# Kernel optimization log

Hardware: AMD Instinct MI355X
Metric: run time of the kernel (lower is better)

## Reference

```python
import jax, jax.numpy as jnp
import numpy as np

S, B, DIN = 3, 4096, 1024
H1, H2, H3, D = 512, 384, 256, 128
K, C = 512, 3            # codebook size, n_codebooks
TEMP = 0.1               # contrastive temperature
EPS = 1e-12


def setup_inputs() -> dict:
    key = jax.random.key(0)
    ks = jax.random.split(key, 16)
    g = lambda k, shp, s=0.05: (jax.random.normal(k, shp, dtype=jnp.float32) * s)
    return {
        'x': jax.random.normal(ks[0], (S, B, DIN), dtype=jnp.float32),
        'enc_w1': g(ks[1], (S, DIN, H1)), 'enc_b1': g(ks[2], (S, H1)),
        'enc_w2': g(ks[3], (S, H1, H2)), 'enc_b2': g(ks[4], (S, H2)),
        'enc_w3': g(ks[5], (S, H2, H3)), 'enc_b3': g(ks[6], (S, H3)),
        'enc_w4': g(ks[7], (S, H3, D)),  'enc_b4': g(ks[8], (S, D)),
        'q_w1': g(ks[9], (D, D)), 'q_b1': g(ks[10], (D,)),
        'q_w2': g(ks[11], (D,)),
        'codebooks': jax.random.normal(ks[12], (C, K, D), dtype=jnp.float32),
    }


def _normalize(v):
    return v / jnp.maximum(jnp.linalg.norm(v, axis=-1, keepdims=True), EPS)


def _forward(x, enc_w1, enc_b1, enc_w2, enc_b2, enc_w3, enc_b3,
             enc_w4, enc_b4, q_w1, q_b1, q_w2, codebooks):
    sg = jax.lax.stop_gradient
    # per-source MLP encoders (stacked over source axis s)
    h = jax.nn.relu(jnp.einsum('sbi,sio->sbo', x, enc_w1) + enc_b1[:, None, :])
    h = jax.nn.relu(jnp.einsum('sbi,sio->sbo', h, enc_w2) + enc_b2[:, None, :])
    h = jax.nn.relu(jnp.einsum('sbi,sio->sbo', h, enc_w3) + enc_b3[:, None, :])
    emb = jnp.einsum('sbi,sio->sbo', h, enc_w4) + enc_b4[:, None, :]  # [S,B,D]

    # attention fusion: Linear->Tanh->Linear(1) per source, softmax over sources
    score = jnp.einsum('sbd,d->sb', jnp.tanh(jnp.einsum('sbd,de->sbe', emb, q_w1) + q_b1), q_w2)
    weight = jax.nn.softmax(score.T, axis=-1)                # [B,S]
    fused = jnp.einsum('bs,sbd->bd', weight, emb)            # [B,D]

    # residual VQ over C codebooks (straight-through, MSE losses)
    res = fused
    q_sum = jnp.zeros_like(fused)
    commit_loss = jnp.float32(0.0)
    for k in range(C):
        e = codebooks[k]                                     # [K,D]
        d2 = (jnp.sum(res * res, axis=1, keepdims=True)
              - 2.0 * res @ e.T + jnp.sum(e * e, axis=1))    # [B,K]
        ids = jnp.argmin(d2, axis=1)
        q = e[ids]                                           # [B,D]
        commit_loss = commit_loss + jnp.mean((sg(q) - res) ** 2)
        q_st = res + sg(q - res)                             # straight-through
        q_sum = q_sum + q_st
        res = res - q_st

    # codebook regularizer: mean pairwise cosine gram of normalized codebooks
    cbn = _normalize(codebooks)
    codebook_loss = jnp.mean(jnp.einsum('mkd,mjd->mkj', cbn, cbn))

    # contrastive losses (projection = identity)
    z1 = _normalize(q_sum)                                   # [B,D]
    contrast = []
    for s in range(S):
        z2 = _normalize(emb[s])
        refl = jnp.exp((z1 @ z1.T) / TEMP)                   # [B,B]
        between = jnp.exp((z1 @ z2.T) / TEMP)
        pos = jnp.diagonal(between)
        denom = refl.sum(1) + between.sum(1) - jnp.diagonal(refl)
        contrast.append(jnp.mean(-jnp.log(pos / denom)))

    return jnp.stack([1.0 * codebook_loss, 0.0 * commit_loss] + contrast)


def reference(x, enc_w1, enc_b1, enc_w2, enc_b2, enc_w3, enc_b3,
              enc_w4, enc_b4, q_w1, q_b1, q_w2, codebooks):
    return _forward(x, enc_w1, enc_b1, enc_w2, enc_b2, enc_w3, enc_b3,
                    enc_w4, enc_b4, q_w1, q_b1, q_w2, codebooks)
```

## Files before the change

### kernel.cpp

```cpp
#include <hip/hip_runtime.h>
#include <hip/hip_bf16.h>

#define S_   3
#define B_   4096
#define DIN_ 1024
#define H1_  512
#define H2_  384
#define H3_  256
#define D_   128
#define K_   512
#define C_   3
#define INV_T 10.0f
#define EPS_  1e-12f
#define EXP10 22026.465794806718f

typedef float f32x4 __attribute__((ext_vector_type(4)));
typedef short bf16x8 __attribute__((ext_vector_type(8)));

__device__ __forceinline__ unsigned short f2bf(float f) {
  unsigned int u = __float_as_uint(f);
  u = (u + 0x7FFF + ((u >> 16) & 1)) >> 16;
  return (unsigned short)u;
}

__device__ __forceinline__ void gl2lds16(const unsigned short* g, unsigned short* l) {
  __builtin_amdgcn_global_load_lds(
      (const __attribute__((address_space(1))) void*)g,
      (__attribute__((address_space(3))) void*)l, 16, 0, 0);
}

__device__ __forceinline__ float waveReduceSum(float v) {
#pragma unroll
  for (int off = 32; off > 0; off >>= 1) v += __shfl_down(v, off, 64);
  return v;
}

__device__ __forceinline__ float waveXorSum(float v) {
#pragma unroll
  for (int off = 32; off > 0; off >>= 1) v += __shfl_xor(v, off, 64);
  return v;
}

__global__ __launch_bounds__(256) void prep_kernel(
    const float* __restrict__ x, unsigned short* __restrict__ xb,
    const float* __restrict__ w1, unsigned short* __restrict__ wt1,
    const float* __restrict__ w2, unsigned short* __restrict__ wt2,
    const float* __restrict__ w3, unsigned short* __restrict__ wt3,
    const float* __restrict__ w4, unsigned short* __restrict__ wt4,
    const float* __restrict__ cb, float* __restrict__ cbn2,
    float* __restrict__ cbsumP, unsigned short* __restrict__ cbb,
    const float* __restrict__ qw1, unsigned short* __restrict__ qw1tb) {
  __shared__ float tt[32][33];
  __shared__ float invn[64];
  const int t = threadIdx.x;
  int blk = blockIdx.x;
  const int NCVT = (S_ * B_ * DIN_) / 1024;
  if (blk < NCVT) {
    int i = (blk * 256 + t) * 4;
    float4 v = *(const float4*)(x + i);
    xb[i + 0] = f2bf(v.x); xb[i + 1] = f2bf(v.y);
    xb[i + 2] = f2bf(v.z); xb[i + 3] = f2bf(v.w);
    return;
  }
  blk -= NCVT;
  const int NT = 1536 + 576 + 288 + 96;
  if (blk >= NT) {
    int cblk = blk - NT;
    if (cblk < 24) {
      const int m = cblk >> 3;
      const int k0 = (cblk & 7) * 64;
      const int w = t >> 6, lane = t & 63;
      for (int r = w * 16; r < w * 16 + 16; r++) {
        int k = k0 + r;
        float2 v = *(const float2*)(cb + ((size_t)m * K_ + k) * D_ + lane * 2);
        unsigned short* crow = cbb + ((size_t)m * K_ + k) * D_;
        crow[lane * 2 + 0] = f2bf(v.x);
        crow[lane * 2 + 1] = f2bf(v.y);
        float n2 = waveXorSum(v.x * v.x + v.y * v.y);
        if (lane == 0) {
          cbn2[m * K_ + k] = n2;
          invn[r] = 1.0f / fmaxf(sqrtf(n2), EPS_);
        }
      }
      __syncthreads();
      if (t < D_) {
        float acc = 0.0f;
        for (int r = 0; r < 64; r++)
          acc += cb[((size_t)m * K_ + k0 + r) * D_ + t] * invn[r];
        cbsumP[(size_t)cblk * D_ + t] = acc;
      }
      return;
    }
    cblk -= 24;
    const int kx = cblk & 3, ny = cblk >> 2;
    const int k0 = kx * 32, n0 = ny * 32;
    const int tx = t & 31, ty = t >> 5;
#pragma unroll
    for (int i = 0; i < 4; i++)
      tt[ty + 8 * i][tx] = qw1[(size_t)(k0 + ty + 8 * i) * D_ + n0 + tx];
    __syncthreads();
#pragma unroll
    for (int i = 0; i < 4; i++)
      qw1tb[(size_t)(n0 + ty + 8 * i) * D_ + k0 + tx] = f2bf(tt[tx][ty + 8 * i]);
    return;
  }
  const float* W; unsigned short* Wt; int K, N;
  if (blk < 1536) { W = w1; Wt = wt1; K = DIN_; N = H1_; }
  else {
    blk -= 1536;
    if (blk < 576) { W = w2; Wt = wt2; K = H1_; N = H2_; }
    else {
      blk -= 576;
      if (blk < 288) { W = w3; Wt = wt3; K = H2_; N = H3_; }
      else { blk -= 288; W = w4; Wt = wt4; K = H3_; N = D_; }
    }
  }
  const int kx_n = K / 32, ny_n = N / 32;
  const int kx = blk % kx_n;
  const int ny = (blk / kx_n) % ny_n;
  const int s  = blk / (kx_n * ny_n);
  const int k0 = kx * 32, n0 = ny * 32;
  const int tx = t & 31, ty = t >> 5;
  const float* Ws = W + (size_t)s * K * N;
  const int nb = N >> 7, kb = K >> 6;
#pragma unroll
  for (int i = 0; i < 4; i++)
    tt[ty + 8 * i][tx] = Ws[(size_t)(k0 + ty + 8 * i) * N + n0 + tx];
  __syncthreads();
  const int k = k0 + tx;
  const int kt = k >> 6, ksl = (k >> 5) & 1;
#pragma unroll
  for (int i = 0; i < 4; i++) {
    int n = n0 + ty + 8 * i;
    size_t dst = ((size_t)(s * nb + (n >> 7)) * kb + kt) * 8192 +
                 (size_t)ksl * 4096 + (size_t)(n & 127) * 32 + (k & 31);
    Wt[dst] = f2bf(tt[tx][ty + 8 * i]);
  }
}

__global__ __launch_bounds__(256) void gemm_lds_kernel(
    const unsigned short* __restrict__ A, const unsigned short* __restrict__ Wsw,
    const float* __restrict__ bias, void* __restrict__ Y,
    int K, int N, int relu, int out_f32) {
  const int t = threadIdx.x;
  const int lane = t & 63;
  const int w = t >> 6;
  const int ln = lane & 15, q = lane >> 4;
  const int wm = w >> 1, wn = w & 1;
  const int n0 = blockIdx.x * 128;
  const int mblk = blockIdx.y;
  const int s = mblk >> 6;
  const int m0 = mblk * 64;
  const int nb = N >> 7, kb = K >> 6;

  const unsigned short* Ag = A + (size_t)m0 * K;
  const unsigned short* Bt = Wsw + ((size_t)(s * nb + blockIdx.x) * kb) * 8192;
  const float* bs = bias + (size_t)s * N;

  __shared__ unsigned short Asm[2 * 64 * 32];
  __shared__ unsigned short Bsm[2 * 8192];

  const int arow0 = t >> 3, ak8 = t & 7;
  const int aL0 = (ak8 >> 2) * 2048 + arow0 * 32 + (ak8 & 3) * 8;
  const size_t gA0 = (size_t)arow0 * K + ak8 * 8;

  bf16x8 ra0 = *(const bf16x8*)(Ag + gA0);
  bf16x8 ra1 = *(const bf16x8*)(Ag + gA0 + (size_t)32 * K);
#pragma unroll
  for (int p = 0; p < 4; p++)
    gl2lds16(Bt + (size_t)(p * 256 + t) * 8, &Bsm[(size_t)(p * 256 + t) * 8]);

  f32x4 acc[2][4];
#pragma unroll
  for (int i = 0; i < 2; i++)
#pragma unroll
    for (int j = 0; j < 4; j++) acc[i][j] = (f32x4){0.f, 0.f, 0.f, 0.f};

  for (int kt = 0; kt < kb; kt++) {
    *(bf16x8*)&Asm[aL0] = ra0;
    *(bf16x8*)&Asm[aL0 + 1024] = ra1;
    __syncthreads();
    const unsigned short* Bcur = &Bsm[(kt & 1) * 8192];
    if (kt + 1 < kb) {
      const unsigned short* Bn = Bt + (size_t)(kt + 1) * 8192;
      unsigned short* Bd = &Bsm[((kt + 1) & 1) * 8192];
#pragma unroll
      for (int p = 0; p < 4; p++)
        gl2lds16(Bn + (size_t)(p * 256 + t) * 8, Bd + (size_t)(p * 256 + t) * 8);
      const size_t g = gA0 + (size_t)(kt + 1) * 64;
      ra0 = *(const bf16x8*)(Ag + g);
      ra1 = *(const bf16x8*)(Ag + g + (size_t)32 * K);
    }
    bf16x8 af[2][2], bf[4][2];
#pragma unroll
    for (int ti = 0; ti < 2; ti++)
#pragma unroll
      for (int ksl = 0; ksl < 2; ksl++)
        af[ti][ksl] = *(const bf16x8*)&Asm[ksl * 2048 + (wm * 32 + ti * 16 + ln) * 32 + q * 8];
#pragma unroll
    for (int tj = 0; tj < 4; tj++)
#pragma unroll
      for (int ksl = 0; ksl < 2; ksl++)
        bf[tj][ksl] = *(const bf16x8*)&Bcur[ksl * 4096 + (wn * 64 + tj * 16 + ln) * 32 + q * 8];
#pragma unroll
    for (int ksl = 0; ksl < 2; ksl++)
#pragma unroll
      for (int ti = 0; ti < 2; ti++)
#pragma unroll
        for (int tj = 0; tj < 4; tj++)
          acc[ti][tj] = __builtin_amdgcn_mfma_f32_16x16x32_bf16(af[ti][ksl], bf[tj][ksl], acc[ti][tj], 0, 0, 0);
    __syncthreads();
  }

#pragma unroll
  for (int ti = 0; ti < 2; ti++)
#pragma unroll
    for (int tj = 0; tj < 4; tj++) {
      const int cc = n0 + wn * 64 + tj * 16 + ln;
      const float bv = bs[cc];
#pragma unroll
      for (int reg = 0; reg < 4; reg++) {
        const int r = m0 + wm * 32 + ti * 16 + q * 4 + reg;
        float v = acc[ti][tj][reg] + bv;
        if (relu) v = fmaxf(v, 0.0f);
        if (out_f32) ((float*)Y)[(size_t)r * N + cc] = v;
        else ((unsigned short*)Y)[(size_t)r * N + cc] = f2bf(v);
      }
    }
}

__global__ __launch_bounds__(512) void scorevq_kernel(
    const float* __restrict__ emb, const unsigned short* __restrict__ qw1tb,
    const float* __restrict__ qb1, const float* __restrict__ qw2,
    const float* __restrict__ cb, const unsigned short* __restrict__ cbb,
    const float* __restrict__ cbn2,
    unsigned short* __restrict__ zb, float* __restrict__ pos) {
  const int b0 = blockIdx.x * 16;
  const int t = threadIdx.x;
  const int w = t >> 6, lane = t & 63;
  const int ln = lane & 15, q = lane >> 4;

  __shared__ float e[48][D_];
  __shared__ unsigned short ebb[48][136];
  __shared__ float qf[16][D_];
  __shared__ float resv[16][D_];
  __shared__ unsigned short resb[16][136];
  __shared__ float red2[8][48];
  __shared__ float sc[48];
  __shared__ float candd[8][16];
  __shared__ int candk[8][16];
  __shared__ int bestk[16];

  bf16x8 bq[4];
  {
    const unsigned short* qp = qw1tb + (size_t)(w * 16 + ln) * D_;
#pragma unroll
    for (int ks = 0; ks < 4; ks++)
      bq[ks] = *(const bf16x8*)(qp + ks * 32 + q * 8);
  }

#pragma unroll
  for (int p = 0; p < 3; p++) {
    int idx = (p * 512 + t) * 4;
    int r = idx >> 7, dd = idx & 127;
    int s = r >> 4, bi = r & 15;
    float4 v = *(const float4*)(emb + ((size_t)(s * B_ + b0 + bi)) * D_ + dd);
    *(float4*)&e[r][dd] = v;
    unsigned int lo = (unsigned int)f2bf(v.x) | ((unsigned int)f2bf(v.y) << 16);
    unsigned int hi = (unsigned int)f2bf(v.z) | ((unsigned int)f2bf(v.w) << 16);
    *(uint2*)&ebb[r][dd] = make_uint2(lo, hi);
  }
  __syncthreads();

  {
    f32x4 sacc[3];
#pragma unroll
    for (int rt = 0; rt < 3; rt++) sacc[rt] = (f32x4){0.f, 0.f, 0.f, 0.f};
#pragma unroll
    for (int ks = 0; ks < 4; ks++) {
#pragma unroll
      for (int rt = 0; rt < 3; rt++) {
        bf16x8 a = *(const bf16x8*)&ebb[rt * 16 + ln][ks * 32 + q * 8];
        sacc[rt] = __builtin_amdgcn_mfma_f32_16x16x32_bf16(a, bq[ks], sacc[rt], 0, 0, 0);
      }
    }
    const int col = w * 16 + ln;
    const float qb = qb1[col], q2v = qw2[col];
#pragma unroll
    for (int rt = 0; rt < 3; rt++)
#pragma unroll
      for (int reg = 0; reg < 4; reg++) {
        float v = tanhf(sacc[rt][reg] + qb) * q2v;
#pragma unroll
        for (int off = 8; off > 0; off >>= 1) v += __shfl_xor(v, off, 16);
        if (ln == 0) red2[w][rt * 16 + q * 4 + reg] = v;
      }
  }
  __syncthreads();
  if (t < 48) {
    float s = 0.f;
#pragma unroll
    for (int ww = 0; ww < 8; ww++) s += red2[ww][t];
    sc[t] = s;
  }
  __syncthreads();

#pragma unroll
  for (int p = 0; p < 4; p++) {
    int idx = p * 512 + t;
    int bi = idx >> 7, dd = idx & 127;
    float s0 = sc[bi], s1 = sc[16 + bi], s2 = sc[32 + bi];
    float mx = fmaxf(s0, fmaxf(s1, s2));
    float e0 = __expf(s0 - mx), e1 = __expf(s1 - mx), e2 = __expf(s2 - mx);
    float inv = 1.0f / (e0 + e1 + e2);
    float fv = (e0 * e[bi][dd] + e1 * e[16 + bi][dd] + e2 * e[32 + bi][dd]) * inv;
    qf[bi][dd] = fv;
    resv[bi][dd] = fv;
    resb[bi][dd] = f2bf(fv);
  }
  __syncthreads();

  for (int c = 0; c < C_; c++) {
    bf16x8 a[4];
#pragma unroll
    for (int ks = 0; ks < 4; ks++)
      a[ks] = *(const bf16x8*)&resb[ln][ks * 32 + q * 8];
    f32x4 acc[4];
#pragma unroll
    for (int tt = 0; tt < 4; tt++) acc[tt] = (f32x4){0.f, 0.f, 0.f, 0.f};
#pragma unroll
    for (int tt = 0; tt < 4; tt++) {
      const int n = w * 64 + tt * 16 + ln;
      const unsigned short* bp = cbb + ((size_t)c * K_ + n) * D_;
#pragma unroll
      for (int ks = 0; ks < 4; ks++) {
        bf16x8 b = *(const bf16x8*)(bp + ks * 32 + q * 8);
        acc[tt] = __builtin_amdgcn_mfma_f32_16x16x32_bf16(a[ks], b, acc[tt], 0, 0, 0);
      }
    }
    float bd[4]; int bk[4];
#pragma unroll
    for (int reg = 0; reg < 4; reg++) { bd[reg] = 3.4e38f; bk[reg] = 0x7fffffff; }
#pragma unroll
    for (int tt = 0; tt < 4; tt++) {
      const int col = w * 64 + tt * 16 + ln;
      const float n2 = cbn2[c * K_ + col];
#pragma unroll
      for (int reg = 0; reg < 4; reg++) {
        float dist = n2 - 2.0f * acc[tt][reg];
        if (dist < bd[reg] || (dist == bd[reg] && col < bk[reg])) { bd[reg] = dist; bk[reg] = col; }
      }
    }
#pragma unroll
    for (int reg = 0; reg < 4; reg++) {
#pragma unroll
      for (int off = 8; off > 0; off >>= 1) {
        float d1 = __shfl_down(bd[reg], off, 16);
        int k1 = __shfl_down(bk[reg], off, 16);
        if (d1 < bd[reg] || (d1 == bd[reg] && k1 < bk[reg])) { bd[reg] = d1; bk[reg] = k1; }
      }
      if (ln == 0) { candd[w][q * 4 + reg] = bd[reg]; candk[w][q * 4 + reg] = bk[reg]; }
    }
    __syncthreads();
    if (w == 0) {
      int row = lane >> 2, g = lane & 3;
      float d0 = candd[2 * g][row]; int k0 = candk[2 * g][row];
      float d1 = candd[2 * g + 1][row]; int k1 = candk[2 * g + 1][row];
      if (d1 < d0 || (d1 == d0 && k1 < k0)) { d0 = d1; k0 = k1; }
#pragma unroll
      for (int off = 2; off > 0; off >>= 1) {
        float dn = __shfl_down(d0, off, 4);
        int kn = __shfl_down(k0, off, 4);
        if (dn < d0 || (dn == d0 && kn < k0)) { d0 = dn; k0 = kn; }
      }
      if (g == 0) bestk[row] = k0;
    }
    __syncthreads();
    {
      int idx = t * 4;
      int r = idx >> 7, dd = idx & 127;
      const float4 qv = *(const float4*)(cb + ((size_t)c * K_ + bestk[r]) * D_ + dd);
      float4 rv = *(float4*)&resv[r][dd];
      rv.x -= qv.x; rv.y -= qv.y; rv.z -= qv.z; rv.w -= qv.w;
      *(float4*)&resv[r][dd] = rv;
      resb[r][dd + 0] = f2bf(rv.x); resb[r][dd + 1] = f2bf(rv.y);
      resb[r][dd + 2] = f2bf(rv.z); resb[r][dd + 3] = f2bf(rv.w);
    }
    __syncthreads();
  }

  {
    int idx = t * 4;
    int r = idx >> 7, dd = idx & 127;
    float4 f = *(float4*)&qf[r][dd];
    float4 rv = *(float4*)&resv[r][dd];
    f.x -= rv.x; f.y -= rv.y; f.z -= rv.z; f.w -= rv.w;
    *(float4*)&qf[r][dd] = f;
  }
  __syncthreads();

#pragma unroll
  for (int rr = 0; rr < 2; rr++) {
    int r = w * 2 + rr;
    float2 v = *(const float2*)&qf[r][lane * 2];
    float n2 = waveXorSum(v.x * v.x + v.y * v.y);
    float inv = 1.0f / fmaxf(sqrtf(n2), EPS_);
    float zx = v.x * inv, zy = v.y * inv;
    zb[(size_t)(b0 + r) * D_ + lane * 2 + 0] = f2bf(zx);
    zb[(size_t)(b0 + r) * D_ + lane * 2 + 1] = f2bf(zy);
    qf[r][lane * 2] = zx; qf[r][lane * 2 + 1] = zy;
  }
  __syncthreads();

#pragma unroll
  for (int rr = 0; rr < 6; rr++) {
    int r = w * 6 + rr;
    int s = r >> 4, bi = r & 15;
    float2 v = *(const float2*)&e[r][lane * 2];
    float n2 = waveXorSum(v.x * v.x + v.y * v.y);
    float inv = 1.0f / fmaxf(sqrtf(n2), EPS_);
    float zx = v.x * inv, zy = v.y * inv;
    size_t gb = (size_t)(1 + s) * B_ + b0 + bi;
    zb[gb * D_ + lane * 2 + 0] = f2bf(zx);
    zb[gb * D_ + lane * 2 + 1] = f2bf(zy);
    float2 a1 = *(const float2*)&qf[bi][lane * 2];
    float dsum = waveXorSum(a1.x * zx + a1.y * zy);
    if (lane == 0) pos[s * B_ + b0 + bi] = dsum;
  }
}

__global__ __launch_bounds__(256) void contrast_mfma_kernel(
    const unsigned short* __restrict__ zb, float* __restrict__ rsP) {
  const int jc = blockIdx.x, ib = blockIdx.y, m = blockIdx.z;
  const int t = threadIdx.x;
  const int w = t >> 6, lane = t & 63;
  const int ln = lane & 15, q = lane >> 4;
  const int i0 = ib * 128 + w * 32;
  const unsigned short* Za = zb;
  const unsigned short* Zm = zb + (size_t)m * B_ * D_;

  __shared__ unsigned short Zsm[64 * 136];

  bf16x8 a[2][4];
#pragma unroll
  for (int si = 0; si < 2; si++)
#pragma unroll
    for (int ks = 0; ks < 4; ks++)
      a[si][ks] = *(const bf16x8*)(Za + (size_t)(i0 + si * 16 + ln) * D_ + ks * 32 + q * 8);

  const unsigned short* tb = Zm + (size_t)(jc * 1024) * D_;
  bf16x8 rz[4];
#pragma unroll
  for (int p = 0; p < 4; p++)
    rz[p] = *(const bf16x8*)(tb + t * 8 + p * 2048);

  float e[2][4] = {};
  for (int jt = 0; jt < 16; jt++) {
#pragma unroll
    for (int p = 0; p < 4; p++) {
      int c = t + p * 256;
      *(bf16x8*)&Zsm[(c >> 4) * 136 + (c & 15) * 8] = rz[p];
    }
    __syncthreads();
    if (jt + 1 < 16) {
      const unsigned short* tn = Zm + (size_t)(jc * 1024 + (jt + 1) * 64) * D_;
#pragma unroll
      for (int p = 0; p < 4; p++)
        rz[p] = *(const bf16x8*)(tn + t * 8 + p * 2048);
    }
    f32x4 acc[2][4];
#pragma unroll
    for (int si = 0; si < 2; si++)
#pragma unroll
      for (int tj = 0; tj < 4; tj++) acc[si][tj] = (f32x4){0.f, 0.f, 0.f, 0.f};
#pragma unroll
    for (int tj = 0; tj < 4; tj++) {
      bf16x8 b[4];
#pragma unroll
      for (int ks = 0; ks < 4; ks++)
        b[ks] = *(const bf16x8*)&Zsm[(tj * 16 + ln) * 136 + ks * 32 + q * 8];
#pragma unroll
      for (int ks = 0; ks < 4; ks++) {
        acc[0][tj] = __builtin_amdgcn_mfma_f32_16x16x32_bf16(a[0][ks], b[ks], acc[0][tj], 0, 0, 0);
        acc[1][tj] = __builtin_amdgcn_mfma_f32_16x16x32_bf16(a[1][ks], b[ks], acc[1][tj], 0, 0, 0);
      }
    }
#pragma unroll
    for (int si = 0; si < 2; si++)
#pragma unroll
      for (int reg = 0; reg < 4; reg++) {
        float s = 0.f;
#pragma unroll
        for (int tj = 0; tj < 4; tj++) s += __expf(acc[si][tj][reg] * INV_T);
        e[si][reg] += s;
      }
    __syncthreads();
  }
#pragma unroll
  for (int si = 0; si < 2; si++)
#pragma unroll
    for (int reg = 0; reg < 4; reg++) {
#pragma unroll
      for (int off = 8; off > 0; off >>= 1)
        e[si][reg] += __shfl_xor(e[si][reg], off, 16);
    }
  if (ln == 0) {
#pragma unroll
    for (int si = 0; si < 2; si++)
#pragma unroll
      for (int reg = 0; reg < 4; reg++)
        rsP[((size_t)m * 4 + jc) * B_ + i0 + si * 16 + q * 4 + reg] = e[si][reg];
  }
}

__global__ __launch_bounds__(256) void final2_kernel(const float* __restrict__ rsP,
                                                     const float* __restrict__ pos,
                                                     const float* __restrict__ cbsumP,
                                                     float* __restrict__ out) {
  const int blk = blockIdx.x;
  const int t = threadIdx.x;
  __shared__ float red[4];
  if (blk == 0) {
    float acc = 0.0f;
    if (t < D_) {
#pragma unroll
      for (int m = 0; m < C_; m++) {
        float v = 0.0f;
#pragma unroll
        for (int b8 = 0; b8 < 8; b8++) v += cbsumP[(size_t)(m * 8 + b8) * D_ + t];
        acc += v * v;
      }
    }
    float v = waveReduceSum(acc);
    if ((t & 63) == 0) red[t >> 6] = v;
    __syncthreads();
    if (t == 0) {
      out[0] = (red[0] + red[1] + red[2] + red[3]) * (1.0f / (3.0f * 512.0f * 512.0f));
      out[1] = 0.0f;
    }
  } else {
    const int s = blk - 1;
    float acc = 0.0f;
    for (int it = 0; it < 16; it++) {
      const int i = it * 256 + t;
      float denom = -EXP10;
#pragma unroll
      for (int jc = 0; jc < 4; jc++) {
        denom += rsP[(size_t)jc * B_ + i];
        denom += rsP[((size_t)(1 + s) * 4 + jc) * B_ + i];
      }
      acc += logf(denom) - pos[s * B_ + i] * INV_T;
    }
    float v = waveReduceSum(acc);
    if ((t & 63) == 0) red[t >> 6] = v;
    __syncthreads();
    if (t == 0)
      out[2 + s] = (red[0] + red[1] + red[2] + red[3]) * (1.0f / 4096.0f);
  }
}

extern "C" void kernel_launch(void* const* d_in, const int* in_sizes, int n_in,
                              void* d_out, int out_size, void* d_ws, size_t ws_size,
                              hipStream_t stream) {
  const float* x    = (const float*)d_in[0];
  const float* w1   = (const float*)d_in[1];
  const float* b1   = (const float*)d_in[2];
  const float* w2   = (const float*)d_in[3];
  const float* b2   = (const float*)d_in[4];
  const float* w3   = (const float*)d_in[5];
  const float* b3   = (const float*)d_in[6];
  const float* w4   = (const float*)d_in[7];
  const float* b4   = (const float*)d_in[8];
  const float* qw1  = (const float*)d_in[9];
  const float* qb1  = (const float*)d_in[10];
  const float* qw2  = (const float*)d_in[11];
  const float* cb   = (const float*)d_in[12];
  float* out = (float*)d_out;
  char* base = (char*)d_ws;

  size_t o = 0;
  auto alloc = [&](size_t bytes) { size_t r = o; o += (bytes + 255) & ~(size_t)255; return r; };
  size_t o_xb   = alloc((size_t)S_ * B_ * DIN_ * 2);
  size_t o_wt1  = alloc((size_t)S_ * H1_ * DIN_ * 2);
  size_t o_wt2  = alloc((size_t)S_ * H2_ * H1_ * 2);
  size_t o_wt3  = alloc((size_t)S_ * H3_ * H2_ * 2);
  size_t o_wt4  = alloc((size_t)S_ * D_ * H3_ * 2);
  size_t o_h1b  = alloc((size_t)S_ * B_ * H1_ * 2);
  size_t o_h2b  = alloc((size_t)S_ * B_ * H2_ * 2);
  size_t o_h3b  = alloc((size_t)S_ * B_ * H3_ * 2);
  size_t o_emb  = alloc((size_t)S_ * B_ * D_ * 4);
  size_t o_zb   = alloc((size_t)4 * B_ * D_ * 2);
  size_t o_cbn2 = alloc((size_t)C_ * K_ * 4);
  size_t o_cbb  = alloc((size_t)C_ * K_ * D_ * 2);
  size_t o_rsP  = alloc((size_t)4 * 4 * B_ * 4);
  size_t o_cbsP = alloc((size_t)C_ * 8 * D_ * 4);
  size_t o_pos  = alloc((size_t)S_ * B_ * 4);
  size_t o_q1t  = alloc((size_t)D_ * D_ * 2);
  (void)ws_size; (void)in_sizes; (void)n_in; (void)out_size;

  unsigned short* xb  = (unsigned short*)(base + o_xb);
  unsigned short* wt1 = (unsigned short*)(base + o_wt1);
  unsigned short* wt2 = (unsigned short*)(base + o_wt2);
  unsigned short* wt3 = (unsigned short*)(base + o_wt3);
  unsigned short* wt4 = (unsigned short*)(base + o_wt4);
  unsigned short* h1b = (unsigned short*)(base + o_h1b);
  unsigned short* h2b = (unsigned short*)(base + o_h2b);
  unsigned short* h3b = (unsigned short*)(base + o_h3b);
  float* emb   = (float*)(base + o_emb);
  unsigned short* zb = (unsigned short*)(base + o_zb);
  float* cbn2  = (float*)(base + o_cbn2);
  unsigned short* cbb = (unsigned short*)(base + o_cbb);
  float* rsP   = (float*)(base + o_rsP);
  float* cbsumP= (float*)(base + o_cbsP);
  float* pos   = (float*)(base + o_pos);
  unsigned short* qw1tb = (unsigned short*)(base + o_q1t);

  const int prep_blocks = (S_ * B_ * DIN_) / 1024 + 1536 + 576 + 288 + 96 + C_ * 8 + 16;
  prep_kernel<<<dim3(prep_blocks), 256, 0, stream>>>(x, xb, w1, wt1, w2, wt2, w3, wt3, w4, wt4,
                                                     cb, cbn2, cbsumP, cbb, qw1, qw1tb);

  const int Mtot = S_ * B_;
  gemm_lds_kernel<<<dim3(H1_ / 128, Mtot / 64), 256, 0, stream>>>(xb, wt1, b1, h1b, DIN_, H1_, 1, 0);
  gemm_lds_kernel<<<dim3(H2_ / 128, Mtot / 64), 256, 0, stream>>>(h1b, wt2, b2, h2b, H1_, H2_, 1, 0);
  gemm_lds_kernel<<<dim3(H3_ / 128, Mtot / 64), 256, 0, stream>>>(h2b, wt3, b3, h3b, H2_, H3_, 1, 0);
  gemm_lds_kernel<<<dim3(D_ / 128, Mtot / 64), 256, 0, stream>>>(h3b, wt4, b4, emb, H3_, D_, 0, 1);

  scorevq_kernel<<<dim3(B_ / 16), 512, 0, stream>>>(emb, qw1tb, qb1, qw2, cb, cbb, cbn2, zb, pos);

  contrast_mfma_kernel<<<dim3(4, 32, 4), 256, 0, stream>>>(zb, rsP);

  final2_kernel<<<dim3(4), 256, 0, stream>>>(rsP, pos, cbsumP, out);
}
```

Measured before the change: 241.1 us.

## Fuse final encoder layer GEMM into score/VQ kernel

Removes the separate fourth-layer GEMM launch and its fp32 emb round trip through global memory. The VQ kernel now loads bf16 h3 rows into LDS and computes the 256->128 projection with MFMA, writing fp32 and bf16 copies of emb directly into shared memory. The prep kernel stores w4 in a plain transposed [s][n][k] bf16 layout for this path. The cost is extra LDS per block (about 25 KB for the h3 tile), which may lower occupancy, and w4 fragments are read straight from global memory without LDS staging.

```diff
diff --git a/kernel.cpp b/kernel.cpp
--- a/kernel.cpp
+++ b/kernel.cpp
@@ -46,7 +46,7 @@
     const float* __restrict__ w1, unsigned short* __restrict__ wt1,
     const float* __restrict__ w2, unsigned short* __restrict__ wt2,
     const float* __restrict__ w3, unsigned short* __restrict__ wt3,
-    const float* __restrict__ w4, unsigned short* __restrict__ wt4,
+    const float* __restrict__ w4, unsigned short* __restrict__ w4tb,
     const float* __restrict__ cb, float* __restrict__ cbn2,
     float* __restrict__ cbsumP, unsigned short* __restrict__ cbb,
     const float* __restrict__ qw1, unsigned short* __restrict__ qw1tb) {
@@ -104,7 +104,7 @@
       qw1tb[(size_t)(n0 + ty + 8 * i) * D_ + k0 + tx] = f2bf(tt[tx][ty + 8 * i]);
     return;
   }
-  const float* W; unsigned short* Wt; int K, N;
+  const float* W; unsigned short* Wt; int K, N; int plain = 0;
   if (blk < 1536) { W = w1; Wt = wt1; K = DIN_; N = H1_; }
   else {
     blk -= 1536;
@@ -112,7 +112,7 @@
     else {
       blk -= 576;
       if (blk < 288) { W = w3; Wt = wt3; K = H2_; N = H3_; }
-      else { blk -= 288; W = w4; Wt = wt4; K = H3_; N = D_; }
+      else { blk -= 288; W = w4; Wt = w4tb; K = H3_; N = D_; plain = 1; }
     }
   }
   const int kx_n = K / 32, ny_n = N / 32;
@@ -128,13 +128,21 @@
     tt[ty + 8 * i][tx] = Ws[(size_t)(k0 + ty + 8 * i) * N + n0 + tx];
   __syncthreads();
   const int k = k0 + tx;
-  const int kt = k >> 6, ksl = (k >> 5) & 1;
-#pragma unroll
-  for (int i = 0; i < 4; i++) {
-    int n = n0 + ty + 8 * i;
-    size_t dst = ((size_t)(s * nb + (n >> 7)) * kb + kt) * 8192 +
-                 (size_t)ksl * 4096 + (size_t)(n & 127) * 32 + (k & 31);
-    Wt[dst] = f2bf(tt[tx][ty + 8 * i]);
+  if (plain) {
+#pragma unroll
+    for (int i = 0; i < 4; i++) {
+      int n = n0 + ty + 8 * i;
+      Wt[((size_t)(s * D_ + n)) * H3_ + k] = f2bf(tt[tx][ty + 8 * i]);
+    }
+  } else {
+    const int kt = k >> 6, ksl = (k >> 5) & 1;
+#pragma unroll
+    for (int i = 0; i < 4; i++) {
+      int n = n0 + ty + 8 * i;
+      size_t dst = ((size_t)(s * nb + (n >> 7)) * kb + kt) * 8192 +
+                   (size_t)ksl * 4096 + (size_t)(n & 127) * 32 + (k & 31);
+      Wt[dst] = f2bf(tt[tx][ty + 8 * i]);
+    }
   }
 }
 
@@ -229,8 +237,9 @@
     }
 }
 
-__global__ __launch_bounds__(512) void scorevq_kernel(
-    const float* __restrict__ emb, const unsigned short* __restrict__ qw1tb,
+__global__ __launch_bounds__(512) void l4vq_kernel(
+    const unsigned short* __restrict__ h3b, const unsigned short* __restrict__ w4tb,
+    const float* __restrict__ b4, const unsigned short* __restrict__ qw1tb,
     const float* __restrict__ qb1, const float* __restrict__ qw2,
     const float* __restrict__ cb, const unsigned short* __restrict__ cbb,
     const float* __restrict__ cbn2,
@@ -240,6 +249,7 @@
   const int w = t >> 6, lane = t & 63;
   const int ln = lane & 15, q = lane >> 4;
 
+  __shared__ unsigned short h3s[48][264];
   __shared__ float e[48][D_];
   __shared__ unsigned short ebb[48][136];
   __shared__ float qf[16][D_];
@@ -261,14 +271,35 @@
 
 #pragma unroll
   for (int p = 0; p < 3; p++) {
-    int idx = (p * 512 + t) * 4;
-    int r = idx >> 7, dd = idx & 127;
+    int f = p * 512 + t;
+    int r = f >> 5, kf = f & 31;
     int s = r >> 4, bi = r & 15;
-    float4 v = *(const float4*)(emb + ((size_t)(s * B_ + b0 + bi)) * D_ + dd);
-    *(float4*)&e[r][dd] = v;
-    unsigned int lo = (unsigned int)f2bf(v.x) | ((unsigned int)f2bf(v.y) << 16);
-    unsigned int hi = (unsigned int)f2bf(v.z) | ((unsigned int)f2bf(v.w) << 16);
-    *(uint2*)&ebb[r][dd] = make_uint2(lo, hi);
+    *(bf16x8*)&h3s[r][kf * 8] =
+        *(const bf16x8*)(h3b + ((size_t)(s * B_ + b0 + bi)) * H3_ + kf * 8);
+  }
+  __syncthreads();
+
+  {
+    const int col = w * 16 + ln;
+#pragma unroll
+    for (int s = 0; s < 3; s++) {
+      f32x4 oacc = (f32x4){0.f, 0.f, 0.f, 0.f};
+      const unsigned short* wp = w4tb + ((size_t)(s * D_ + col)) * H3_;
+#pragma unroll
+      for (int ks = 0; ks < 8; ks++) {
+        bf16x8 bfrag = *(const bf16x8*)(wp + ks * 32 + q * 8);
+        bf16x8 afrag = *(const bf16x8*)&h3s[s * 16 + ln][ks * 32 + q * 8];
+        oacc = __builtin_amdgcn_mfma_f32_16x16x32_bf16(afrag, bfrag, oacc, 0, 0, 0);
+      }
+      const float bv = b4[s * D_ + col];
+#pragma unroll
+      for (int reg = 0; reg < 4; reg++) {
+        int r = s * 16 + q * 4 + reg;
+        float v = oacc[reg] + bv;
+        e[r][col] = v;
+        ebb[r][col] = f2bf(v);
+      }
+    }
   }
   __syncthreads();
 
@@ -584,11 +615,10 @@
   size_t o_wt1  = alloc((size_t)S_ * H1_ * DIN_ * 2);
   size_t o_wt2  = alloc((size_t)S_ * H2_ * H1_ * 2);
   size_t o_wt3  = alloc((size_t)S_ * H3_ * H2_ * 2);
-  size_t o_wt4  = alloc((size_t)S_ * D_ * H3_ * 2);
+  size_t o_w4t  = alloc((size_t)S_ * D_ * H3_ * 2);
   size_t o_h1b  = alloc((size_t)S_ * B_ * H1_ * 2);
   size_t o_h2b  = alloc((size_t)S_ * B_ * H2_ * 2);
   size_t o_h3b  = alloc((size_t)S_ * B_ * H3_ * 2);
-  size_t o_emb  = alloc((size_t)S_ * B_ * D_ * 4);
   size_t o_zb   = alloc((size_t)4 * B_ * D_ * 2);
   size_t o_cbn2 = alloc((size_t)C_ * K_ * 4);
   size_t o_cbb  = alloc((size_t)C_ * K_ * D_ * 2);
@@ -602,11 +632,10 @@
   unsigned short* wt1 = (unsigned short*)(base + o_wt1);
   unsigned short* wt2 = (unsigned short*)(base + o_wt2);
   unsigned short* wt3 = (unsigned short*)(base + o_wt3);
-  unsigned short* wt4 = (unsigned short*)(base + o_wt4);
+  unsigned short* w4tb= (unsigned short*)(base + o_w4t);
   unsigned short* h1b = (unsigned short*)(base + o_h1b);
   unsigned short* h2b = (unsigned short*)(base + o_h2b);
   unsigned short* h3b = (unsigned short*)(base + o_h3b);
-  float* emb   = (float*)(base + o_emb);
   unsigned short* zb = (unsigned short*)(base + o_zb);
   float* cbn2  = (float*)(base + o_cbn2);
   unsigned short* cbb = (unsigned short*)(base + o_cbb);
@@ -616,16 +645,16 @@
   unsigned short* qw1tb = (unsigned short*)(base + o_q1t);
 
   const int prep_blocks = (S_ * B_ * DIN_) / 1024 + 1536 + 576 + 288 + 96 + C_ * 8 + 16;
-  prep_kernel<<<dim3(prep_blocks), 256, 0, stream>>>(x, xb, w1, wt1, w2, wt2, w3, wt3, w4, wt4,
+  prep_kernel<<<dim3(prep_blocks), 256, 0, stream>>>(x, xb, w1, wt1, w2, wt2, w3, wt3, w4, w4tb,
                                                      cb, cbn2, cbsumP, cbb, qw1, qw1tb);
 
   const int Mtot = S_ * B_;
   gemm_lds_kernel<<<dim3(H1_ / 128, Mtot / 64), 256, 0, stream>>>(xb, wt1, b1, h1b, DIN_, H1_, 1, 0);
   gemm_lds_kernel<<<dim3(H2_ / 128, Mtot / 64), 256, 0, stream>>>(h1b, wt2, b2, h2b, H1_, H2_, 1, 0);
   gemm_lds_kernel<<<dim3(H3_ / 128, Mtot / 64), 256, 0, stream>>>(h2b, wt3, b3, h3b, H2_, H3_, 1, 0);
-  gemm_lds_kernel<<<dim3(D_ / 128, Mtot / 64), 256, 0, stream>>>(h3b, wt4, b4, emb, H3_, D_, 0, 1);
-
-  scorevq_kernel<<<dim3(B_ / 16), 512, 0, stream>>>(emb, qw1tb, qb1, qw2, cb, cbb, cbn2, zb, pos);
+
+  l4vq_kernel<<<dim3(B_ / 16), 512, 0, stream>>>(h3b, w4tb, b4, qw1tb, qb1, qw2,
+                                                 cb, cbb, cbn2, zb, pos);
 
   contrast_mfma_kernel<<<dim3(4, 32, 4), 256, 0, stream>>>(zb, rsP);
 
```

After: 240.1 us. Within noise of the previous version (-0.4%).
